# Kernel optimization log

Hardware: AMD Instinct MI355X
Metric: run time of the kernel (lower is better)

The kernel has to match this reference:

```python
import jax, jax.numpy as jnp
import numpy as np

N_ORDER = 256
DT = 1.0 / 512.0


def _hippo_legt_mats(N, dt):
    # Continuous-time LegT transition (same as `transition` in the source).
    Q = np.arange(N, dtype=np.float64)
    R = (2 * Q + 1)[:, None]
    j, i = np.meshgrid(Q, Q)
    A = np.where(i < j, -1.0, (-1.0) ** (i - j + 1)) * R
    B = (-1.0) ** Q[:, None] * R  # (N, 1)
    # scipy cont2discrete(..., method='bilinear') == GBT with alpha=0.5:
    #   Ad = (I - dt/2 A)^{-1} (I + dt/2 A),  Bd = (I - dt/2 A)^{-1} (dt B)
    I = np.eye(N)
    ema = I - (dt / 2.0) * A
    Ad = np.linalg.solve(ema, I + (dt / 2.0) * A)
    Bd = np.linalg.solve(ema, dt * B).squeeze(-1)  # (N,)
    return Ad.astype(np.float32), Bd.astype(np.float32)


def setup_inputs() -> dict:
    key = jax.random.key(0)
    inputs = jax.random.normal(key, (8, 128, 512), dtype=jnp.float32)  # (batch, D, L)
    Ad, Bd = _hippo_legt_mats(N_ORDER, DT)
    return {"inputs": inputs, "A": jnp.asarray(Ad), "B": jnp.asarray(Bd)}


def reference(inputs, A, B):
    # inputs: (batch, D, L); A: (N, N); B: (N,)
    # c_t = c_{t-1} @ A^T + f_t * B,  output stacked over t: (L, batch, D, N)
    N = A.shape[0]
    c0 = jnp.zeros(inputs.shape[:-1] + (N,), dtype=inputs.dtype)  # (batch, D, N)
    fs = jnp.moveaxis(inputs, -1, 0)  # (L, batch, D)

    def step(c, f):
        c_new = c @ A.T + f[..., None] * B  # (batch, D, N)
        return c_new, c_new

    _, cs = jax.lax.scan(step, c0, fs)  # (L, batch, D, N)
    return cs
```

## Files before the change

kernel.cpp:

```cpp
#include <hip/hip_runtime.h>
#include <stdint.h>


typedef _Float16 half8 __attribute__((ext_vector_type(8)));
typedef float floatx4 __attribute__((ext_vector_type(4)));


__global__ void k_at(const float* __restrict__ A, float* __restrict__ At,
                     const float* __restrict__ Bvec, float* __restrict__ Vbuf) {
    int i = blockIdx.x, j = threadIdx.x;
    At[j * 256 + i] = A[i * 256 + j];
    if (i == 0) Vbuf[j] = Bvec[j];
}

__global__ void k_g8(const float* __restrict__ inp, _Float16* __restrict__ g8) {
    int bd = blockIdx.x;
    const float* f = inp + (size_t)bd * 512;
    _Float16* g = g8 + (size_t)bd * 5248;
    for (int idx = threadIdx.x; idx < 5248; idx += 256) {
        int r = idx / 656;
        int i = idx - r * 656;
        int jj = i + r;
        float val = (jj < 512) ? f[511 - jj] : 0.f;
        g[idx] = (_Float16)val;
    }
}

__global__ __launch_bounds__(1024) void k_level(
    const float* __restrict__ M, const float* __restrict__ Mt,
    float* __restrict__ C, float* __restrict__ Ct,
    float* __restrict__ Vbuf, int m, int do_sq)
{
    __shared__ float vec[256];
    __shared__ float part[3][256];
    const int tid = threadIdx.x;
    const int r  = tid & 255;
    const int kc = tid >> 8;
    const int b  = blockIdx.x;
    const bool sq = (do_sq && b < 256);
    const int j = do_sq ? (b - 256) : b;
    const float* Msrc;
    if (sq) {
        if (kc == 0) vec[r] = M[b * 256 + r];
        Msrc = M;
    } else {
        if (kc == 0) vec[r] = Vbuf[j * 256 + r];
        Msrc = Mt;
    }
    __syncthreads();
    const float* Mp = Msrc + (size_t)(kc * 64) * 256 + r;
    const float* vp = vec + kc * 64;
    float acc = 0.f;
#pragma unroll 8
    for (int k = 0; k < 64; ++k) acc += vp[k] * Mp[(size_t)k * 256];
    if (kc) part[kc - 1][r] = acc;
    __syncthreads();
    if (kc == 0) {
        acc += part[0][r] + part[1][r] + part[2][r];
        if (sq) {
            C[b * 256 + r]  = acc;
            Ct[r * 256 + b] = acc;
        } else {
            Vbuf[(m + j) * 256 + r] = acc;
        }
    }
}

__global__ void k_vt(const float* __restrict__ Vbuf, _Float16* __restrict__ Vt) {
    int n = threadIdx.x;
    int k0 = blockIdx.x * 8;
    half8 wv;
#pragma unroll
    for (int i = 0; i < 8; ++i) wv[i] = (_Float16)Vbuf[(size_t)(k0 + i) * 256 + n];
    *reinterpret_cast<half8*>(Vt + (size_t)n * 512 + k0) = wv;
}

__global__ __launch_bounds__(256, 2) void k_main(
    const _Float16* __restrict__ g8,
    const _Float16* __restrict__ Vt,
    float* __restrict__ out)
{
    __shared__ _Float16 ldsA[8 * 656];
    __shared__ _Float16 ldsB[2][256 * 40];

    const int tid  = threadIdx.x;
    const int lane = tid & 63;
    const int w    = tid >> 6;
    const int bd   = blockIdx.x & 1023;
    const int tt   = blockIdx.x >> 10;
    const int t0   = 384 - 128 * tt;
    const int Kmax = t0 + 128;

    {
        const uint4* gsrc = reinterpret_cast<const uint4*>(g8 + (size_t)bd * 5248);
        uint4* adst = reinterpret_cast<uint4*>(ldsA);
        for (int idx = tid; idx < 656; idx += 256) adst[idx] = gsrc[idx];
    }

    const int wave_mt = (w & 1) << 6;
    const int wave_nn = (w >> 1) << 7;
    const int m16  = lane & 15;
    const int quad = lane >> 4;
    const int hi8  = quad << 3;

    int abase[4];
#pragma unroll
    for (int mf = 0; mf < 4; ++mf) {
        int t_lane = t0 + wave_mt + mf * 16 + m16;
        int c = 511 - t_lane;
        int rsh = (c + hi8) & 7;
        abase[mf] = rsh * 1312 + 2 * (hi8 + c - rsh);
    }
    int bbase[8];
#pragma unroll
    for (int bf = 0; bf < 8; ++bf) {
        int n_row = wave_nn + bf * 16 + m16;
        bbase[bf] = n_row * 80 + hi8 * 2;
    }

    const int srow = tid >> 2;
    const int scol = tid & 3;
    const _Float16* vbase = Vt + (size_t)srow * 512 + scol * 8;

    uint4 st[4];
#pragma unroll
    for (int rr = 0; rr < 4; ++rr)
        st[rr] = *reinterpret_cast<const uint4*>(vbase + (size_t)rr * 64 * 512);
#pragma unroll
    for (int rr = 0; rr < 4; ++rr)
        *reinterpret_cast<uint4*>(reinterpret_cast<char*>(&ldsB[0][0])
                                  + (srow + rr * 64) * 80 + scol * 16) = st[rr];

    floatx4 acc[4][8];
#pragma unroll
    for (int mf = 0; mf < 4; ++mf)
#pragma unroll
        for (int bf = 0; bf < 8; ++bf) {
            floatx4 z = {0.f, 0.f, 0.f, 0.f};
            acc[mf][bf] = z;
        }

    int cur = 0;
    for (int k0 = 0; k0 < Kmax; k0 += 32) {
        const bool more = (k0 + 32 < Kmax);
        if (more) {
#pragma unroll
            for (int rr = 0; rr < 4; ++rr)
                st[rr] = *reinterpret_cast<const uint4*>(
                    vbase + (size_t)rr * 64 * 512 + (k0 + 32));
        }
        __syncthreads();

        half8 a[4], b[8];
        const char* aptr = reinterpret_cast<const char*>(ldsA) + 2 * k0;
#pragma unroll
        for (int mf = 0; mf < 4; ++mf)
            a[mf] = *reinterpret_cast<const half8*>(aptr + abase[mf]);
        const char* bptr = reinterpret_cast<const char*>(&ldsB[cur][0]);
#pragma unroll
        for (int bf = 0; bf < 8; ++bf)
            b[bf] = *reinterpret_cast<const half8*>(bptr + bbase[bf]);

#pragma unroll
        for (int mf = 0; mf < 4; ++mf)
#pragma unroll
            for (int bf = 0; bf < 8; ++bf)
                acc[mf][bf] = __builtin_amdgcn_mfma_f32_16x16x32_f16(
                    a[mf], b[bf], acc[mf][bf], 0, 0, 0);

        if (more) {
            char* wdst = reinterpret_cast<char*>(&ldsB[cur ^ 1][0]);
#pragma unroll
            for (int rr = 0; rr < 4; ++rr)
                *reinterpret_cast<uint4*>(wdst + (srow + rr * 64) * 80 + scol * 16) = st[rr];
        }
        cur ^= 1;
    }

#pragma unroll
    for (int mf = 0; mf < 4; ++mf) {
        int trow0 = t0 + wave_mt + mf * 16 + quad * 4;
#pragma unroll
        for (int bf = 0; bf < 8; ++bf) {
            int n = wave_nn + bf * 16 + m16;
#pragma unroll
            for (int reg = 0; reg < 4; ++reg) {
                int t = trow0 + reg;
                out[(size_t)t * 262144 + (size_t)bd * 256 + n] = acc[mf][bf][reg];
            }
        }
    }
}


extern "C" void kernel_launch(void* const* d_in, const int* in_sizes, int n_in,
                              void* d_out, int out_size, void* d_ws, size_t ws_size,
                              hipStream_t stream) {
    const float* inputs = (const float*)d_in[0];
    const float* A      = (const float*)d_in[1];
    const float* Bvec   = (const float*)d_in[2];
    float* out = (float*)d_out;

    float* At   = (float*)d_ws;
    float* M0   = At  + 65536;
    float* M0t  = M0  + 65536;
    float* M1   = M0t + 65536;
    float* M1t  = M1  + 65536;
    float* Vbuf = M1t + 65536;
    _Float16* Vt = (_Float16*)(Vbuf + 131072);
    _Float16* g8 = Vt + 131072;

    k_g8 <<<1024, 256, 0, stream>>>(inputs, g8);
    k_at <<<256, 256, 0, stream>>>(A, At, Bvec, Vbuf);
    k_level<<<257, 1024, 0, stream>>>(A,  At,  M0, M0t, Vbuf,   1, 1);
    k_level<<<258, 1024, 0, stream>>>(M0, M0t, M1, M1t, Vbuf,   2, 1);
    k_level<<<260, 1024, 0, stream>>>(M1, M1t, M0, M0t, Vbuf,   4, 1);
    k_level<<<264, 1024, 0, stream>>>(M0, M0t, M1, M1t, Vbuf,   8, 1);
    k_level<<<272, 1024, 0, stream>>>(M1, M1t, M0, M0t, Vbuf,  16, 1);
    k_level<<<288, 1024, 0, stream>>>(M0, M0t, M1, M1t, Vbuf,  32, 1);
    k_level<<<320, 1024, 0, stream>>>(M1, M1t, M0, M0t, Vbuf,  64, 1);
    k_level<<<384, 1024, 0, stream>>>(M0, M0t, M1, M1t, Vbuf, 128, 1);
    k_level<<<256, 1024, 0, stream>>>(M1, M1t, M0, M0t, Vbuf, 256, 0);
    k_vt  <<<64, 256, 0, stream>>>(Vbuf, Vt);
    k_main<<<4096, 256, 0, stream>>>(g8, Vt, out);
}
```

Measured before the change: 725.5 us.

## Load B fragments directly from global in MFMA layout, drop LDS staging

Repacks the precomputed V matrix into a k-blocked fp16 layout that matches MFMA B-fragment order, so each wave loads its fragments straight from global memory into registers. This removes the LDS double buffer for B and the per-iteration block barrier, and unrolls the K loop by two with register double-buffering of both A and B fragments. MFMA sections are wrapped in s_setprio to favor issue. The trade is redundant global/L2 loads across waves sharing the same B columns, and global load latency is now hidden only by one register stage.

```diff
diff --git a/kernel.cpp b/kernel.cpp
--- a/kernel.cpp
+++ b/kernel.cpp
@@ -66,22 +66,21 @@
     }
 }
 
-__global__ void k_vt(const float* __restrict__ Vbuf, _Float16* __restrict__ Vt) {
+__global__ void k_vb(const float* __restrict__ Vbuf, _Float16* __restrict__ Vb) {
     int n = threadIdx.x;
-    int k0 = blockIdx.x * 8;
+    int kb = blockIdx.x;
     half8 wv;
 #pragma unroll
-    for (int i = 0; i < 8; ++i) wv[i] = (_Float16)Vbuf[(size_t)(k0 + i) * 256 + n];
-    *reinterpret_cast<half8*>(Vt + (size_t)n * 512 + k0) = wv;
+    for (int j = 0; j < 8; ++j) wv[j] = (_Float16)Vbuf[(size_t)(kb * 8 + j) * 256 + n];
+    *reinterpret_cast<half8*>(Vb + (size_t)kb * 2048 + n * 8) = wv;
 }
 
 __global__ __launch_bounds__(256, 2) void k_main(
     const _Float16* __restrict__ g8,
-    const _Float16* __restrict__ Vt,
+    const _Float16* __restrict__ Vb,
     float* __restrict__ out)
 {
     __shared__ _Float16 ldsA[8 * 656];
-    __shared__ _Float16 ldsB[2][256 * 40];
 
     const int tid  = threadIdx.x;
     const int lane = tid & 63;
@@ -111,25 +110,12 @@
         int rsh = (c + hi8) & 7;
         abase[mf] = rsh * 1312 + 2 * (hi8 + c - rsh);
     }
-    int bbase[8];
+    int bidx[8];
 #pragma unroll
     for (int bf = 0; bf < 8; ++bf) {
         int n_row = wave_nn + bf * 16 + m16;
-        bbase[bf] = n_row * 80 + hi8 * 2;
-    }
-
-    const int srow = tid >> 2;
-    const int scol = tid & 3;
-    const _Float16* vbase = Vt + (size_t)srow * 512 + scol * 8;
-
-    uint4 st[4];
-#pragma unroll
-    for (int rr = 0; rr < 4; ++rr)
-        st[rr] = *reinterpret_cast<const uint4*>(vbase + (size_t)rr * 64 * 512);
-#pragma unroll
-    for (int rr = 0; rr < 4; ++rr)
-        *reinterpret_cast<uint4*>(reinterpret_cast<char*>(&ldsB[0][0])
-                                  + (srow + rr * 64) * 80 + scol * 16) = st[rr];
+        bidx[bf] = quad * 2048 + n_row * 8;
+    }
 
     floatx4 acc[4][8];
 #pragma unroll
@@ -140,41 +126,57 @@
             acc[mf][bf] = z;
         }
 
-    int cur = 0;
-    for (int k0 = 0; k0 < Kmax; k0 += 32) {
-        const bool more = (k0 + 32 < Kmax);
-        if (more) {
-#pragma unroll
-            for (int rr = 0; rr < 4; ++rr)
-                st[rr] = *reinterpret_cast<const uint4*>(
-                    vbase + (size_t)rr * 64 * 512 + (k0 + 32));
-        }
-        __syncthreads();
-
-        half8 a[4], b[8];
-        const char* aptr = reinterpret_cast<const char*>(ldsA) + 2 * k0;
+    half8 aA[4], aB[4], bA[8], bB[8];
+
+#pragma unroll
+    for (int bf = 0; bf < 8; ++bf)
+        bA[bf] = *reinterpret_cast<const half8*>(Vb + bidx[bf]);
+
+    __syncthreads();
+
+    const char* aptr0 = reinterpret_cast<const char*>(ldsA);
+#pragma unroll
+    for (int mf = 0; mf < 4; ++mf)
+        aA[mf] = *reinterpret_cast<const half8*>(aptr0 + abase[mf]);
+
+    for (int k0 = 0; k0 < Kmax; k0 += 64) {
+        {
+            const _Float16* vb = Vb + ((size_t)(k0 + 32) << 8);
+#pragma unroll
+            for (int bf = 0; bf < 8; ++bf)
+                bB[bf] = *reinterpret_cast<const half8*>(vb + bidx[bf]);
+            const char* ap = aptr0 + 2 * (k0 + 32);
+#pragma unroll
+            for (int mf = 0; mf < 4; ++mf)
+                aB[mf] = *reinterpret_cast<const half8*>(ap + abase[mf]);
+        }
+        __builtin_amdgcn_s_setprio(1);
 #pragma unroll
         for (int mf = 0; mf < 4; ++mf)
-            a[mf] = *reinterpret_cast<const half8*>(aptr + abase[mf]);
-        const char* bptr = reinterpret_cast<const char*>(&ldsB[cur][0]);
-#pragma unroll
-        for (int bf = 0; bf < 8; ++bf)
-            b[bf] = *reinterpret_cast<const half8*>(bptr + bbase[bf]);
-
+#pragma unroll
+            for (int bf = 0; bf < 8; ++bf)
+                acc[mf][bf] = __builtin_amdgcn_mfma_f32_16x16x32_f16(
+                    aA[mf], bA[bf], acc[mf][bf], 0, 0, 0);
+        __builtin_amdgcn_s_setprio(0);
+
+        if (k0 + 64 < Kmax) {
+            const _Float16* vb = Vb + ((size_t)(k0 + 64) << 8);
+#pragma unroll
+            for (int bf = 0; bf < 8; ++bf)
+                bA[bf] = *reinterpret_cast<const half8*>(vb + bidx[bf]);
+            const char* ap = aptr0 + 2 * (k0 + 64);
+#pragma unroll
+            for (int mf = 0; mf < 4; ++mf)
+                aA[mf] = *reinterpret_cast<const half8*>(ap + abase[mf]);
+        }
+        __builtin_amdgcn_s_setprio(1);
 #pragma unroll
         for (int mf = 0; mf < 4; ++mf)
 #pragma unroll
             for (int bf = 0; bf < 8; ++bf)
                 acc[mf][bf] = __builtin_amdgcn_mfma_f32_16x16x32_f16(
-                    a[mf], b[bf], acc[mf][bf], 0, 0, 0);
-
-        if (more) {
-            char* wdst = reinterpret_cast<char*>(&ldsB[cur ^ 1][0]);
-#pragma unroll
-            for (int rr = 0; rr < 4; ++rr)
-                *reinterpret_cast<uint4*>(wdst + (srow + rr * 64) * 80 + scol * 16) = st[rr];
-        }
-        cur ^= 1;
+                    aB[mf], bB[bf], acc[mf][bf], 0, 0, 0);
+        __builtin_amdgcn_s_setprio(0);
     }
 
 #pragma unroll
@@ -207,8 +209,8 @@
     float* M1   = M0t + 65536;
     float* M1t  = M1  + 65536;
     float* Vbuf = M1t + 65536;
-    _Float16* Vt = (_Float16*)(Vbuf + 131072);
-    _Float16* g8 = Vt + 131072;
+    _Float16* Vb = (_Float16*)(Vbuf + 131072);
+    _Float16* g8 = Vb + 131072;
 
     k_g8 <<<1024, 256, 0, stream>>>(inputs, g8);
     k_at <<<256, 256, 0, stream>>>(A, At, Bvec, Vbuf);
@@ -221,6 +223,6 @@
     k_level<<<320, 1024, 0, stream>>>(M1, M1t, M0, M0t, Vbuf,  64, 1);
     k_level<<<384, 1024, 0, stream>>>(M0, M0t, M1, M1t, Vbuf, 128, 1);
     k_level<<<256, 1024, 0, stream>>>(M1, M1t, M0, M0t, Vbuf, 256, 0);
-    k_vt  <<<64, 256, 0, stream>>>(Vbuf, Vt);
-    k_main<<<4096, 256, 0, stream>>>(g8, Vt, out);
-}
+    k_vb  <<<64, 256, 0, stream>>>(Vbuf, Vb);
+    k_main<<<4096, 256, 0, stream>>>(g8, Vb, out);
+}
```

Result: faster. 617.8 us (-14.8%).
